# Optimization experiments

Measured on AMD Instinct MI355X. Metric: run time of the kernel, lower is better.

Reference implementation:

```python
import jax, jax.numpy as jnp
import numpy as np

# Log-signature at depth m=3, d channels, expressed in the full tensor basis
# (iisignature 'expanded' convention; the Lyndon-basis output of method '' is a
# fixed linear projection of these coefficients).

def _chen_step(carry, dx):
    # carry: signature levels S1 [B,d], S2 [B,d,d], S3 [B,d,d,d]
    # dx: increment of one segment, [B,d]. Segment signature E = exp(dx).
    S1, S2, S3 = carry
    E2 = 0.5 * jnp.einsum('bi,bj->bij', dx, dx)
    E3 = (1.0 / 6.0) * jnp.einsum('bi,bj,bk->bijk', dx, dx, dx)
    nS1 = S1 + dx
    nS2 = S2 + jnp.einsum('bi,bj->bij', S1, dx) + E2
    nS3 = (S3
           + jnp.einsum('bij,bk->bijk', S2, dx)
           + jnp.einsum('bi,bjk->bijk', S1, E2)
           + E3)
    return (nS1, nS2, nS3), None


def _logsig(x):
    # x: [B, L, d] path. Returns expanded log-signature [B, d + d^2 + d^3].
    B, L, d = x.shape
    dx = jnp.swapaxes(x[:, 1:] - x[:, :-1], 0, 1)  # [L-1, B, d]
    init = (jnp.zeros((B, d), x.dtype),
            jnp.zeros((B, d, d), x.dtype),
            jnp.zeros((B, d, d, d), x.dtype))
    (S1, S2, S3), _ = jax.lax.scan(_chen_step, init, dx)
    # log(1 + S) truncated at level 3 in the tensor algebra
    l1 = S1
    l2 = S2 - 0.5 * jnp.einsum('bi,bj->bij', S1, S1)
    l3 = (S3
          - 0.5 * (jnp.einsum('bi,bjk->bijk', S1, S2)
                   + jnp.einsum('bij,bk->bijk', S2, S1))
          + (1.0 / 3.0) * jnp.einsum('bi,bj,bk->bijk', S1, S1, S1))
    return jnp.concatenate(
        [l1.reshape(B, -1), l2.reshape(B, -1), l3.reshape(B, -1)], axis=-1)


def setup_inputs() -> dict:
    key = jax.random.key(0)
    B, L, d = 2048, 256, 8
    steps = 0.1 * jax.random.normal(key, (B, L, d), dtype=jnp.float32)
    x = jnp.cumsum(steps, axis=1)  # random-walk paths keep signatures well-scaled
    return {"x": x}


def reference(x):
    return _logsig(x)
```

## Files before the change

kernel.cpp:

```cpp
#include <hip/hip_runtime.h>


#define LEN 256
#define DCH 8
#define NW 4
#define CHUNK 64
#define TPAD 260
#define OUTSTRIDE (DCH + DCH*DCH + DCH*DCH*DCH)

__global__ __launch_bounds__(256) void logsig_fused(const float* __restrict__ x,
                                                    float* __restrict__ out) {
    __shared__ __align__(16) float dxT[DCH][TPAD];
    __shared__ __align__(16) float sig1[NW][8];
    __shared__ __align__(16) float sig2[NW][64];
    __shared__ __align__(16) float sig3[NW][512];
    __shared__ __align__(16) float s1buf[8];
    __shared__ __align__(16) float s2buf[64];

    const int tid  = threadIdx.x;
    const int w    = tid >> 6;
    const int lane = tid & 63;
    const int i    = lane >> 3;
    const int j    = lane & 7;
    const int b    = blockIdx.x;

    const float4* x4 = (const float4*)(x + (size_t)b * (LEN * DCH));
    for (int f = tid; f < 512; f += 256) {
        float4 dv;
        if (f < 510) {
            float4 a = x4[f];
            float4 c = x4[f + 2];
            dv.x = c.x - a.x; dv.y = c.y - a.y; dv.z = c.z - a.z; dv.w = c.w - a.w;
        } else {
            dv.x = 0.f; dv.y = 0.f; dv.z = 0.f; dv.w = 0.f;
        }
        int t  = f >> 1;
        int c0 = (f & 1) * 4;
        dxT[c0 + 0][t] = dv.x;
        dxT[c0 + 1][t] = dv.y;
        dxT[c0 + 2][t] = dv.z;
        dxT[c0 + 3][t] = dv.w;
    }
    __syncthreads();

    float h1 = 0.f, s2 = 0.f;
    float s3[8];
#pragma unroll
    for (int k = 0; k < 8; ++k) s3[k] = 0.f;

    const float c6 = 1.f / 6.f;
    const float* vip = &dxT[i][w * CHUNK];
    const float* vjp = &dxT[j][w * CHUNK];
    const float* rvp = &dxT[lane & 7][w * CHUNK + (lane >> 3)];

#define STEP(DXI, DXJ, U)                                                     \
    do {                                                                      \
        float dxi = (DXI), dxj = (DXJ);                                       \
        float r0 = __int_as_float(__builtin_amdgcn_readlane(rv, 8*(U)+0));    \
        float r1 = __int_as_float(__builtin_amdgcn_readlane(rv, 8*(U)+1));    \
        float r2 = __int_as_float(__builtin_amdgcn_readlane(rv, 8*(U)+2));    \
        float r3 = __int_as_float(__builtin_amdgcn_readlane(rv, 8*(U)+3));    \
        float r4 = __int_as_float(__builtin_amdgcn_readlane(rv, 8*(U)+4));    \
        float r5 = __int_as_float(__builtin_amdgcn_readlane(rv, 8*(U)+5));    \
        float r6 = __int_as_float(__builtin_amdgcn_readlane(rv, 8*(U)+6));    \
        float r7 = __int_as_float(__builtin_amdgcn_readlane(rv, 8*(U)+7));    \
        float h1n = fmaf(0.5f, dxi, h1);                    \
        float uu  = h1 + h1n;                              \
        float tt  = fmaf(c6, dxi, h1);                    \
        float w3  = fmaf(tt, dxj, s2);                                        \
        s3[0] = fmaf(w3, r0, s3[0]);                                          \
        s3[1] = fmaf(w3, r1, s3[1]);                                          \
        s3[2] = fmaf(w3, r2, s3[2]);                                          \
        s3[3] = fmaf(w3, r3, s3[3]);                                          \
        s3[4] = fmaf(w3, r4, s3[4]);                                          \
        s3[5] = fmaf(w3, r5, s3[5]);                                          \
        s3[6] = fmaf(w3, r6, s3[6]);                                          \
        s3[7] = fmaf(w3, r7, s3[7]);                                          \
        s2 = fmaf(uu, dxj, s2);                                               \
        h1 = h1n;                                                             \
    } while (0)

    for (int tb = 0; tb < CHUNK; tb += 8) {
        int rv = __float_as_int(rvp[tb]);
        float4 vi0 = *(const float4*)(vip + tb);
        float4 vi1 = *(const float4*)(vip + tb + 4);
        float4 vj0 = *(const float4*)(vjp + tb);
        float4 vj1 = *(const float4*)(vjp + tb + 4);
        STEP(vi0.x, vj0.x, 0);
        STEP(vi0.y, vj0.y, 1);
        STEP(vi0.z, vj0.z, 2);
        STEP(vi0.w, vj0.w, 3);
        STEP(vi1.x, vj1.x, 4);
        STEP(vi1.y, vj1.y, 5);
        STEP(vi1.z, vj1.z, 6);
        STEP(vi1.w, vj1.w, 7);
    }
#undef STEP

    float s1 = h1 + h1;

    if (j == 0) sig1[w][i] = s1;
    sig2[w][lane] = s2;
    float* sp = &sig3[w][lane * 8];
    *(float4*)(sp)     = make_float4(s3[0], s3[1], s3[2], s3[3]);
    *(float4*)(sp + 4) = make_float4(s3[4], s3[5], s3[6], s3[7]);
    __syncthreads();

    if (w != 0) return;

    for (int c = 1; c < NW; ++c) {
        float B1i  = sig1[c][i];
        float B1j  = sig1[c][j];
        float B2ij = sig2[c][lane];
        float4 b1a = *(const float4*)&sig1[c][0];
        float4 b1b = *(const float4*)&sig1[c][4];
        const float* b2row = &sig2[c][j * 8];
        float4 b2a = *(const float4*)(b2row);
        float4 b2b = *(const float4*)(b2row + 4);
        const float* b3row = &sig3[c][lane * 8];
        float4 b3a = *(const float4*)(b3row);
        float4 b3b = *(const float4*)(b3row + 4);
        float B1k[8]  = {b1a.x, b1a.y, b1a.z, b1a.w, b1b.x, b1b.y, b1b.z, b1b.w};
        float B2jk[8] = {b2a.x, b2a.y, b2a.z, b2a.w, b2b.x, b2b.y, b2b.z, b2b.w};
        float B3[8]   = {b3a.x, b3a.y, b3a.z, b3a.w, b3b.x, b3b.y, b3b.z, b3b.w};
#pragma unroll
        for (int k = 0; k < 8; ++k)
            s3[k] = s3[k] + B3[k] + s1 * B2jk[k] + s2 * B1k[k];
        s2 = s2 + B2ij + s1 * B1j;
        s1 = s1 + B1i;
    }

    if (j == 0) s1buf[i] = s1;
    s2buf[lane] = s2;

    float S1r[8], S2rj[8];
#pragma unroll
    for (int k = 0; k < 8; ++k) S1r[k] = s1buf[k];
#pragma unroll
    for (int k = 0; k < 8; ++k) S2rj[k] = s2buf[j * 8 + k];
    float s1j = s1buf[j];

    float* ob = out + (size_t)b * OUTSTRIDE;
    if (lane < 8) ob[lane] = s1buf[lane];
    ob[8 + lane] = fmaf(-0.5f * s1, s1j, s2);

    float c3 = (1.f / 3.f) * s1 * s1j;
    float l3[8];
#pragma unroll
    for (int k = 0; k < 8; ++k)
        l3[k] = s3[k] - 0.5f * (s1 * S2rj[k] + s2 * S1r[k]) + c3 * S1r[k];
    float* p3 = ob + 72 + lane * 8;
    *(float4*)(p3)     = make_float4(l3[0], l3[1], l3[2], l3[3]);
    *(float4*)(p3 + 4) = make_float4(l3[4], l3[5], l3[6], l3[7]);
}

extern "C" void kernel_launch(void* const* d_in, const int* in_sizes, int n_in,
                              void* d_out, int out_size, void* d_ws, size_t ws_size,
                              hipStream_t stream) {
    const float* x = (const float*)d_in[0];
    float* out = (float*)d_out;
    const int B = in_sizes[0] / (LEN * DCH);
    hipLaunchKernelGGL(logsig_fused, dim3(B), dim3(256), 0, stream, x, out);
}
```

Measured before the change: 77.29 us.

## Use summation by parts on raw path points loaded via scalar loads

Rewrites the level-3 accumulation by summation by parts. It multiplies weight differences (w3p - w3) by the raw path values x[t] instead of the increments dx[t]. The x values are fetched with s_load_dwordx16 into scalar registers, replacing the eight readlane broadcasts per step, and a boundary term is added after the loop. The level-2 update is also reformulated. The risks are the inline asm that waits on lgkmcnt(0) every iteration, which serializes the scalar loads, and possible floating-point rounding changes from the reformulation.

After: 82.46 us. 6.7% more time.

```diff
diff --git a/kernel.cpp b/kernel.cpp
--- a/kernel.cpp
+++ b/kernel.cpp
@@ -7,6 +7,9 @@
 #define CHUNK 64
 #define TPAD 260
 #define OUTSTRIDE (DCH + DCH*DCH + DCH*DCH*DCH)
+
+typedef int v16i __attribute__((ext_vector_type(16)));
+typedef int v8i  __attribute__((ext_vector_type(8)));
 
 __global__ __launch_bounds__(256) void logsig_fused(const float* __restrict__ x,
                                                     float* __restrict__ out) {
@@ -43,59 +46,66 @@
     }
     __syncthreads();
 
-    float h1 = 0.f, s2 = 0.f;
+    const int uw = __builtin_amdgcn_readfirstlane(w);
+    const float* xch = x + (size_t)b * (LEN * DCH) + uw * (CHUNK * DCH);
+
+    float h1 = 0.f, s2 = 0.f, w3p = 0.f;
     float s3[8];
 #pragma unroll
     for (int k = 0; k < 8; ++k) s3[k] = 0.f;
 
     const float c6 = 1.f / 6.f;
-    const float* vip = &dxT[i][w * CHUNK];
-    const float* vjp = &dxT[j][w * CHUNK];
-    const float* rvp = &dxT[lane & 7][w * CHUNK + (lane >> 3)];
+    const float* vip = &dxT[i][uw * CHUNK];
+    const float* vjp = &dxT[j][uw * CHUNK];
 
-#define STEP(DXI, DXJ, U)                                                     \
+#define STEP(DXI, DXJ, RV, O)                                                 \
     do {                                                                      \
         float dxi = (DXI), dxj = (DXJ);                                       \
-        float r0 = __int_as_float(__builtin_amdgcn_readlane(rv, 8*(U)+0));    \
-        float r1 = __int_as_float(__builtin_amdgcn_readlane(rv, 8*(U)+1));    \
-        float r2 = __int_as_float(__builtin_amdgcn_readlane(rv, 8*(U)+2));    \
-        float r3 = __int_as_float(__builtin_amdgcn_readlane(rv, 8*(U)+3));    \
-        float r4 = __int_as_float(__builtin_amdgcn_readlane(rv, 8*(U)+4));    \
-        float r5 = __int_as_float(__builtin_amdgcn_readlane(rv, 8*(U)+5));    \
-        float r6 = __int_as_float(__builtin_amdgcn_readlane(rv, 8*(U)+6));    \
-        float r7 = __int_as_float(__builtin_amdgcn_readlane(rv, 8*(U)+7));    \
         float h1n = fmaf(0.5f, dxi, h1);                    \
-        float uu  = h1 + h1n;                              \
         float tt  = fmaf(c6, dxi, h1);                    \
         float w3  = fmaf(tt, dxj, s2);                                        \
-        s3[0] = fmaf(w3, r0, s3[0]);                                          \
-        s3[1] = fmaf(w3, r1, s3[1]);                                          \
-        s3[2] = fmaf(w3, r2, s3[2]);                                          \
-        s3[3] = fmaf(w3, r3, s3[3]);                                          \
-        s3[4] = fmaf(w3, r4, s3[4]);                                          \
-        s3[5] = fmaf(w3, r5, s3[5]);                                          \
-        s3[6] = fmaf(w3, r6, s3[6]);                                          \
-        s3[7] = fmaf(w3, r7, s3[7]);                                          \
-        s2 = fmaf(uu, dxj, s2);                                               \
-        h1 = h1n;                                                             \
+        float wd  = w3p - w3;                                                 \
+        s3[0] = fmaf(wd, __int_as_float((RV)[(O) + 0]), s3[0]);               \
+        s3[1] = fmaf(wd, __int_as_float((RV)[(O) + 1]), s3[1]);               \
+        s3[2] = fmaf(wd, __int_as_float((RV)[(O) + 2]), s3[2]);               \
+        s3[3] = fmaf(wd, __int_as_float((RV)[(O) + 3]), s3[3]);               \
+        s3[4] = fmaf(wd, __int_as_float((RV)[(O) + 4]), s3[4]);               \
+        s3[5] = fmaf(wd, __int_as_float((RV)[(O) + 5]), s3[5]);               \
+        s3[6] = fmaf(wd, __int_as_float((RV)[(O) + 6]), s3[6]);               \
+        s3[7] = fmaf(wd, __int_as_float((RV)[(O) + 7]), s3[7]);               \
+        float tt2 = fmaf(c6, dxi, tt);                    \
+        s2 = fmaf(tt2, dxj, w3);                     \
+        h1 = h1n; w3p = w3;                                                   \
     } while (0)
 
-    for (int tb = 0; tb < CHUNK; tb += 8) {
-        int rv = __float_as_int(rvp[tb]);
-        float4 vi0 = *(const float4*)(vip + tb);
-        float4 vi1 = *(const float4*)(vip + tb + 4);
-        float4 vj0 = *(const float4*)(vjp + tb);
-        float4 vj1 = *(const float4*)(vjp + tb + 4);
-        STEP(vi0.x, vj0.x, 0);
-        STEP(vi0.y, vj0.y, 1);
-        STEP(vi0.z, vj0.z, 2);
-        STEP(vi0.w, vj0.w, 3);
-        STEP(vi1.x, vj1.x, 4);
-        STEP(vi1.y, vj1.y, 5);
-        STEP(vi1.z, vj1.z, 6);
-        STEP(vi1.w, vj1.w, 7);
+    for (int g = 0; g < 16; ++g) {
+        v16i ra, rb;
+        const float* gp = xch + g * 32;
+        asm volatile("s_load_dwordx16 %0, %2, 0\n\t"
+                     "s_load_dwordx16 %1, %2, 64\n\t"
+                     "s_waitcnt lgkmcnt(0)"
+                     : "=s"(ra), "=s"(rb) : "s"(gp));
+        float4 vi = *(const float4*)(vip + g * 4);
+        float4 vj = *(const float4*)(vjp + g * 4);
+        STEP(vi.x, vj.x, ra, 0);
+        STEP(vi.y, vj.y, ra, 8);
+        STEP(vi.z, vj.z, rb, 0);
+        STEP(vi.w, vj.w, rb, 8);
     }
 #undef STEP
+
+    {
+        int rt = uw * CHUNK + CHUNK;
+        if (rt > LEN - 1) rt = LEN - 1;
+        const float* bp = x + (size_t)b * (LEN * DCH) + rt * DCH;
+        v8i rc;
+        asm volatile("s_load_dwordx8 %0, %1, 0\n\t"
+                     "s_waitcnt lgkmcnt(0)"
+                     : "=s"(rc) : "s"(bp));
+#pragma unroll
+        for (int k = 0; k < 8; ++k)
+            s3[k] = fmaf(w3p, __int_as_float(rc[k]), s3[k]);
+    }
 
     float s1 = h1 + h1;
 
```
